# Performance work log

Measured on AMD Instinct MI355X. Metric: run time of the kernel, lower is better.

## Reference

```python
import jax, jax.numpy as jnp
import numpy as np

N = 4096          # neurons (and input size)
T = 300           # timesteps = time / dt
DT = 1.0
TIME = 300.0
REST = 0.0
RESET = 0.0
THRESH = 10.0
REFRAC = 1.0
TC_DECAY = 100.0


def setup_inputs() -> dict:
    key = jax.random.key(0)
    k1, k2, k3 = jax.random.split(key, 3)
    inp = jax.random.randint(k1, (T, N), 0, 2).astype(jnp.int32)   # binary spike train
    w = jax.random.normal(k2, (N, N), jnp.float32) * 0.05
    w_rec = jax.random.normal(k3, (N, N), jnp.float32) * 0.05
    return {"inp": inp, "w": w, "w_rec": w_rec}


def _simulate(inp, w, w_rec):
    # Faithful port of LIFLayer.__call__ applied over T timesteps via lax.scan.
    # Per step (original order): x = inp@w + s_prev@w_rec; v = decay*(v-rest)+rest;
    # x[rt>0]=0; rt-=dt; v+=x; s=(v>=thresh); t[s]=ts*dt/time; rt[s]=refrac; v[s]=reset.
    decay = jnp.exp(jnp.float32(-DT / TC_DECAY))
    n = w.shape[1]
    v0 = jnp.full((n,), RESET, jnp.float32)
    rt0 = jnp.zeros((n,), jnp.float32)
    s0 = jnp.zeros((n,), jnp.float32)   # previous-step spikes (s[:, -1])
    t0 = jnp.ones((n,), jnp.float32)    # t initialized to ones (store_all_spikes=False)

    def step(carry, xs):
        v, rt, s_prev, t_prev = carry
        inp_t, ts = xs
        x = inp_t.astype(jnp.float32) @ w + s_prev @ w_rec   # [n]
        v = decay * (v - REST) + REST                        # v_ext = 0 (default)
        x = jnp.where(rt > 0, jnp.float32(0.0), x)           # refractory gating
        rt = rt - DT
        v = v + x
        spike = v >= THRESH
        s = spike.astype(jnp.float32)
        t_new = jnp.where(spike, ts.astype(jnp.float32) * DT / TIME, t_prev)
        rt = jnp.where(spike, jnp.float32(REFRAC), rt)
        v = jnp.where(spike, jnp.float32(RESET), v)
        return (v, rt, s, t_new), (s, t_new, v)

    _, (s_all, t_all, v_all) = jax.lax.scan(
        step, (v0, rt0, s0, t0), (inp, jnp.arange(inp.shape[0]))
    )
    return s_all, t_all, v_all


def reference(inp, w, w_rec):
    # Returns per-timestep spikes [T,n], spike-time record [T,n], and membrane
    # potential trace [T,n] (post-reset v, the internal state the kernel computes).
    return _simulate(inp, w, w_rec)
```

## Files before the change

### kernel.cpp

```cpp
#include <hip/hip_runtime.h>
#include <hip/hip_cooperative_groups.h>

namespace cg = cooperative_groups;

#define NN    4096
#define TT    300
#define TPAD  320
#define TCH   20
#define GRID  256
#define BLOCK 1024
#define NREP  16
#define WSTRIDE 18
#define HROWS 2048
#define DECAYF 0.9900498337491681f
#define THRESHF 10.0f

#define WLDS_BYTES (HROWS * WSTRIDE * 4)
#define DSM_BYTES  (WLDS_BYTES + 2 * 16 * 17 * 4)

#define WS_REQ ((size_t)NN*TPAD*4*2 + (size_t)NREP*2*256*4)

__device__ __forceinline__ uint4 llc_load_v4(const uint4* p) {
    uint4 r;
    asm volatile("global_load_dwordx4 %0, %1, off sc0 sc1\n\t"
                 "s_waitcnt vmcnt(0)"
                 : "=v"(r) : "v"(p) : "memory");
    return r;
}

__global__ __launch_bounds__(BLOCK, 4)
void lif_sim(const int* __restrict__ inp, const float* __restrict__ w,
             const float* __restrict__ w_rec, float* __restrict__ out,
             float* __restrict__ ws)
{
    float* inpT = ws;
    float* X    = ws + (size_t)NN * TPAD;
    unsigned int* maskrep = (unsigned int*)(X + (size_t)TPAD * NN);

    float* s_all = out;
    float* t_all = out + (size_t)TT * NN;
    float* v_all = out + (size_t)2 * TT * NN;

    cg::grid_group grid = cg::this_grid();
    const int tid  = threadIdx.x;
    const int bid  = blockIdx.x;
    const int gtid = bid * BLOCK + tid;

    extern __shared__ __align__(16) unsigned char dsm[];
    float*        smem    = (float*)dsm;
    float*        wlds    = (float*)dsm;
    float*        red_sh  = (float*)(dsm + WLDS_BYTES);

    if (gtid < NREP * 2 * 256) maskrep[gtid] = 0u;
    if (gtid < NN * 32) {
        int j = gtid >> 5, tl = gtid & 31;
        if (tl < TPAD - TT) inpT[(size_t)j * TPAD + TT + tl] = 0.0f;
    }
    for (int idx = gtid; idx < TT * NN; idx += GRID * BLOCK) {
        int t = idx >> 12, j = idx & (NN - 1);
        inpT[(size_t)j * TPAD + t] = (float)inp[idx];
    }
    grid.sync();

    {
        const int ct  = bid >> 4;
        const int cc  = bid & 15;
        const int c1  = tid & 255;
        const int jp  = tid >> 8;
        const int col = cc * 256 + c1;
        const int t0  = ct * TCH;
        const int j0  = jp * 1024;
        const float* wp = w + col;
        float acc[20];
#pragma unroll
        for (int k = 0; k < 20; ++k) acc[k] = 0.0f;
        for (int j = j0; j < j0 + 1024; ++j) {
            float wj = wp[(size_t)j * NN];
            const float* iprow = inpT + (size_t)j * TPAD + t0;
#pragma unroll
            for (int k = 0; k < 20; ++k) acc[k] = fmaf(iprow[k], wj, acc[k]);
        }
#pragma unroll
        for (int half = 0; half < 2; ++half) {
#pragma unroll
            for (int k = 0; k < 10; ++k) smem[(jp * 10 + k) * 256 + c1] = acc[half * 10 + k];
            __syncthreads();
            if (jp == 0) {
#pragma unroll
                for (int k = 0; k < 10; ++k) {
                    float s = smem[k * 256 + c1] + smem[(10 + k) * 256 + c1]
                            + smem[(20 + k) * 256 + c1] + smem[(30 + k) * 256 + c1];
                    X[(size_t)(t0 + half * 10 + k) * NN + col] = s;
                }
            }
            __syncthreads();
        }
    }
    grid.sync();

    const int colgrp = ((bid & 7) << 5) | (bid >> 3);
    const int col0   = colgrp * 16;
    const int lane = tid & 63;
    const int wave = tid >> 6;
    const int c    = tid & 15;
    const int r    = tid >> 4;
    const int col  = col0 + c;

    {
        const int srow = tid >> 2;
        const int c4   = (tid & 3) << 2;
#pragma unroll
        for (int pass = 0; pass < 8; ++pass) {
            const int row = pass * 256 + srow;
            const float4 q = *(const float4*)(w_rec + (size_t)row * NN + col0 + c4);
            float2* dst = (float2*)(wlds + row * WSTRIDE + c4);
            dst[0] = make_float2(q.x, q.y);
            dst[1] = make_float2(q.z, q.w);
        }
    }
    __syncthreads();

    float v = 0.0f, tv = 1.0f;
    int sprev = 0;
    const float* wrc = w_rec + col + (size_t)(r << 6) * NN;
    const int ldsbase = (r << 6) * WSTRIDE + c;
    unsigned int* myrep = maskrep + ((bid & 15) * 2) * 256;

    float xreg = 0.0f;
    if (tid < 16) xreg = X[col];

    for (int t = 0; t < TT; ++t) {
        const uint4* pp = (const uint4*)(myrep + (t & 1) * 256) + r;
        const unsigned int ut = (unsigned int)t;
        uint4 q;
        for (;;) {
            q = llc_load_v4(pp);
            unsigned int bad = ((q.x >> 16) ^ ut) | ((q.y >> 16) ^ ut)
                             | ((q.z >> 16) ^ ut) | ((q.w >> 16) ^ ut);
            if (__all(bad == 0u)) break;
        }
        unsigned long long M = ((unsigned long long)(q.x & 0xFFFFu))
                             | ((unsigned long long)(q.y & 0xFFFFu) << 16)
                             | ((unsigned long long)(q.z & 0xFFFFu) << 32)
                             | ((unsigned long long)(q.w & 0xFFFFu) << 48);

        float acc0 = 0.0f, acc1 = 0.0f, acc2 = 0.0f, acc3 = 0.0f;
        if (r < 32) {
            while (M) {
                float l0, l1 = 0.0f, l2 = 0.0f, l3 = 0.0f;
                int b0 = __builtin_ctzll(M); M &= M - 1;
                l0 = wlds[ldsbase + b0 * WSTRIDE];
                if (M) { int b = __builtin_ctzll(M); M &= M - 1; l1 = wlds[ldsbase + b * WSTRIDE]; }
                if (M) { int b = __builtin_ctzll(M); M &= M - 1; l2 = wlds[ldsbase + b * WSTRIDE]; }
                if (M) { int b = __builtin_ctzll(M); M &= M - 1; l3 = wlds[ldsbase + b * WSTRIDE]; }
                acc0 += l0 + l2; acc1 += l1 + l3;
            }
        } else {
            while (M) {
                float l0,        l1 = 0.0f, l2 = 0.0f, l3 = 0.0f,
                      l4 = 0.0f, l5 = 0.0f, l6 = 0.0f, l7 = 0.0f,
                      l8 = 0.0f, l9 = 0.0f, l10 = 0.0f, l11 = 0.0f,
                      l12 = 0.0f, l13 = 0.0f, l14 = 0.0f, l15 = 0.0f;
                int b0 = __builtin_ctzll(M); M &= M - 1;
                l0 = wrc[(size_t)b0 * NN];
                if (M) { int b = __builtin_ctzll(M); M &= M - 1; l1  = wrc[(size_t)b * NN]; }
                if (M) { int b = __builtin_ctzll(M); M &= M - 1; l2  = wrc[(size_t)b * NN]; }
                if (M) { int b = __builtin_ctzll(M); M &= M - 1; l3  = wrc[(size_t)b * NN]; }
                if (M) { int b = __builtin_ctzll(M); M &= M - 1; l4  = wrc[(size_t)b * NN]; }
                if (M) { int b = __builtin_ctzll(M); M &= M - 1; l5  = wrc[(size_t)b * NN]; }
                if (M) { int b = __builtin_ctzll(M); M &= M - 1; l6  = wrc[(size_t)b * NN]; }
                if (M) { int b = __builtin_ctzll(M); M &= M - 1; l7  = wrc[(size_t)b * NN]; }
                if (M) { int b = __builtin_ctzll(M); M &= M - 1; l8  = wrc[(size_t)b * NN]; }
                if (M) { int b = __builtin_ctzll(M); M &= M - 1; l9  = wrc[(size_t)b * NN]; }
                if (M) { int b = __builtin_ctzll(M); M &= M - 1; l10 = wrc[(size_t)b * NN]; }
                if (M) { int b = __builtin_ctzll(M); M &= M - 1; l11 = wrc[(size_t)b * NN]; }
                if (M) { int b = __builtin_ctzll(M); M &= M - 1; l12 = wrc[(size_t)b * NN]; }
                if (M) { int b = __builtin_ctzll(M); M &= M - 1; l13 = wrc[(size_t)b * NN]; }
                if (M) { int b = __builtin_ctzll(M); M &= M - 1; l14 = wrc[(size_t)b * NN]; }
                if (M) { int b = __builtin_ctzll(M); M &= M - 1; l15 = wrc[(size_t)b * NN]; }
                acc0 += l0 + l4;  acc1 += l1 + l5;  acc2 += l2 + l6;  acc3 += l3 + l7;
                acc0 += l8 + l12; acc1 += l9 + l13; acc2 += l10 + l14; acc3 += l11 + l15;
            }
        }
        float part = (acc0 + acc1) + (acc2 + acc3);
        part += __shfl_xor(part, 16, 64);
        part += __shfl_xor(part, 32, 64);
        float* red = red_sh + (t & 1) * (16 * 17);
        if (lane < 16) red[wave * 17 + lane] = part;
        __syncthreads();

        if (wave == 0) {
            const int cw = lane & 15, h = lane >> 4;
            const float* sp = red + h * 4 * 17 + cw;
            float s = (sp[0] + sp[17]) + (sp[34] + sp[51]);
            s += __shfl_xor(s, 16, 64);
            s += __shfl_xor(s, 32, 64);

            bool spike = false;
            if (lane < 16) {
                float x = xreg + s;
                v *= DECAYF;
                if (sprev) x = 0.0f;
                v += x;
                spike = v >= THRESHF;
                if (spike) { tv = (float)t * (1.0f / 300.0f); v = 0.0f; }
                sprev = spike ? 1 : 0;
            }
            unsigned long long bal = __ballot(spike);
            unsigned int word = ((unsigned int)(t + 1) << 16)
                              | (unsigned int)(bal & 0xFFFFull);
            const int par = (t + 1) & 1;
            if (lane < NREP)
                __hip_atomic_store(maskrep + (lane * 2 + par) * 256 + colgrp, word,
                                   __ATOMIC_RELAXED, __HIP_MEMORY_SCOPE_AGENT);
            if (lane < 16) {
                size_t o = (size_t)t * NN + col;
                __builtin_nontemporal_store(spike ? 1.0f : 0.0f, &s_all[o]);
                __builtin_nontemporal_store(tv, &t_all[o]);
                __builtin_nontemporal_store(v, &v_all[o]);
                if (t + 1 < TT)
                    xreg = __builtin_nontemporal_load(&X[(size_t)(t + 1) * NN + col]);
            }
        }
    }
}

extern "C" void kernel_launch(void* const* d_in, const int* in_sizes, int n_in,
                              void* d_out, int out_size, void* d_ws, size_t ws_size,
                              hipStream_t stream) {
    if (ws_size < WS_REQ) return;
    const int*   inp   = (const int*)d_in[0];
    const float* w     = (const float*)d_in[1];
    const float* w_rec = (const float*)d_in[2];
    float* out = (float*)d_out;
    float* ws  = (float*)d_ws;
    hipFuncSetAttribute((const void*)lif_sim,
                        hipFuncAttributeMaxDynamicSharedMemorySize, DSM_BYTES);
    void* args[] = {(void*)&inp, (void*)&w, (void*)&w_rec, (void*)&out, (void*)&ws};
    hipLaunchCooperativeKernel((const void*)lif_sim, dim3(GRID), dim3(BLOCK),
                               args, DSM_BYTES, stream);
}
```

Before: 2.008 ms.

## Poll spike mask with one wave and broadcast via LDS; unroll LDS gather

Only wave 0 now spins on the replicated spike-mask words in the last-level cache and copies them to shared memory, followed by a block barrier. The other 15 waves no longer issue their own polling loads, which cuts memory traffic and contention on the flag lines. This adds a __syncthreads per step and single-buffers the reduction scratch. The change also raises wave 0's priority during the spike/flag-publish section, replaces the agent-scope atomic store with an sc0 sc1 store, and widens the LDS gather unroll from 4 to 8.

```diff
diff --git a/kernel.cpp b/kernel.cpp
--- a/kernel.cpp
+++ b/kernel.cpp
@@ -16,7 +16,7 @@
 #define THRESHF 10.0f
 
 #define WLDS_BYTES (HROWS * WSTRIDE * 4)
-#define DSM_BYTES  (WLDS_BYTES + 2 * 16 * 17 * 4)
+#define DSM_BYTES  (WLDS_BYTES + 1024 + 16 * 17 * 4)
 
 #define WS_REQ ((size_t)NN*TPAD*4*2 + (size_t)NREP*2*256*4)
 
@@ -26,6 +26,11 @@
                  "s_waitcnt vmcnt(0)"
                  : "=v"(r) : "v"(p) : "memory");
     return r;
+}
+
+__device__ __forceinline__ void llc_store_u32(unsigned int* p, unsigned int v) {
+    asm volatile("global_store_dword %0, %1, off sc0 sc1"
+                 :: "v"(p), "v"(v) : "memory");
 }
 
 __global__ __launch_bounds__(BLOCK, 4)
@@ -49,7 +54,8 @@
     extern __shared__ __align__(16) unsigned char dsm[];
     float*        smem    = (float*)dsm;
     float*        wlds    = (float*)dsm;
-    float*        red_sh  = (float*)(dsm + WLDS_BYTES);
+    unsigned int* mask_sh = (unsigned int*)(dsm + WLDS_BYTES);
+    float*        red_sh  = (float*)(dsm + WLDS_BYTES + 1024);
 
     if (gtid < NREP * 2 * 256) maskrep[gtid] = 0u;
     if (gtid < NN * 32) {
@@ -130,30 +136,43 @@
     if (tid < 16) xreg = X[col];
 
     for (int t = 0; t < TT; ++t) {
-        const uint4* pp = (const uint4*)(myrep + (t & 1) * 256) + r;
-        const unsigned int ut = (unsigned int)t;
-        uint4 q;
-        for (;;) {
-            q = llc_load_v4(pp);
-            unsigned int bad = ((q.x >> 16) ^ ut) | ((q.y >> 16) ^ ut)
-                             | ((q.z >> 16) ^ ut) | ((q.w >> 16) ^ ut);
-            if (__all(bad == 0u)) break;
-        }
-        unsigned long long M = ((unsigned long long)(q.x & 0xFFFFu))
-                             | ((unsigned long long)(q.y & 0xFFFFu) << 16)
-                             | ((unsigned long long)(q.z & 0xFFFFu) << 32)
-                             | ((unsigned long long)(q.w & 0xFFFFu) << 48);
-
+        if (wave == 0) {
+            const uint4* pp = (const uint4*)(myrep + (t & 1) * 256) + lane;
+            const unsigned int ut = (unsigned int)t;
+            uint4 q;
+            for (;;) {
+                q = llc_load_v4(pp);
+                unsigned int bad = ((q.x >> 16) ^ ut) | ((q.y >> 16) ^ ut)
+                                 | ((q.z >> 16) ^ ut) | ((q.w >> 16) ^ ut);
+                if (__all(bad == 0u)) break;
+            }
+            ((uint4*)mask_sh)[lane] = q;
+        }
+        __syncthreads();
+
+        unsigned long long M;
+        {
+            const unsigned int* ms = mask_sh + (r << 2);
+            M = ((unsigned long long)(ms[0] & 0xFFFFu))
+              | ((unsigned long long)(ms[1] & 0xFFFFu) << 16)
+              | ((unsigned long long)(ms[2] & 0xFFFFu) << 32)
+              | ((unsigned long long)(ms[3] & 0xFFFFu) << 48);
+        }
         float acc0 = 0.0f, acc1 = 0.0f, acc2 = 0.0f, acc3 = 0.0f;
         if (r < 32) {
             while (M) {
-                float l0, l1 = 0.0f, l2 = 0.0f, l3 = 0.0f;
+                float l0, l1 = 0.0f, l2 = 0.0f, l3 = 0.0f,
+                      l4 = 0.0f, l5 = 0.0f, l6 = 0.0f, l7 = 0.0f;
                 int b0 = __builtin_ctzll(M); M &= M - 1;
                 l0 = wlds[ldsbase + b0 * WSTRIDE];
                 if (M) { int b = __builtin_ctzll(M); M &= M - 1; l1 = wlds[ldsbase + b * WSTRIDE]; }
                 if (M) { int b = __builtin_ctzll(M); M &= M - 1; l2 = wlds[ldsbase + b * WSTRIDE]; }
                 if (M) { int b = __builtin_ctzll(M); M &= M - 1; l3 = wlds[ldsbase + b * WSTRIDE]; }
-                acc0 += l0 + l2; acc1 += l1 + l3;
+                if (M) { int b = __builtin_ctzll(M); M &= M - 1; l4 = wlds[ldsbase + b * WSTRIDE]; }
+                if (M) { int b = __builtin_ctzll(M); M &= M - 1; l5 = wlds[ldsbase + b * WSTRIDE]; }
+                if (M) { int b = __builtin_ctzll(M); M &= M - 1; l6 = wlds[ldsbase + b * WSTRIDE]; }
+                if (M) { int b = __builtin_ctzll(M); M &= M - 1; l7 = wlds[ldsbase + b * WSTRIDE]; }
+                acc0 += l0 + l4; acc1 += l1 + l5; acc2 += l2 + l6; acc3 += l3 + l7;
             }
         } else {
             while (M) {
@@ -185,13 +204,13 @@
         float part = (acc0 + acc1) + (acc2 + acc3);
         part += __shfl_xor(part, 16, 64);
         part += __shfl_xor(part, 32, 64);
-        float* red = red_sh + (t & 1) * (16 * 17);
-        if (lane < 16) red[wave * 17 + lane] = part;
+        if (lane < 16) red_sh[wave * 17 + lane] = part;
         __syncthreads();
 
         if (wave == 0) {
+            __builtin_amdgcn_s_setprio(1);
             const int cw = lane & 15, h = lane >> 4;
-            const float* sp = red + h * 4 * 17 + cw;
+            const float* sp = red_sh + h * 4 * 17 + cw;
             float s = (sp[0] + sp[17]) + (sp[34] + sp[51]);
             s += __shfl_xor(s, 16, 64);
             s += __shfl_xor(s, 32, 64);
@@ -211,8 +230,8 @@
                               | (unsigned int)(bal & 0xFFFFull);
             const int par = (t + 1) & 1;
             if (lane < NREP)
-                __hip_atomic_store(maskrep + (lane * 2 + par) * 256 + colgrp, word,
-                                   __ATOMIC_RELAXED, __HIP_MEMORY_SCOPE_AGENT);
+                llc_store_u32(maskrep + (lane * 2 + par) * 256 + colgrp, word);
+            __builtin_amdgcn_s_setprio(0);
             if (lane < 16) {
                 size_t o = (size_t)t * NN + col;
                 __builtin_nontemporal_store(spike ? 1.0f : 0.0f, &s_all[o]);
```

Result: faster. 1.699 ms (-15.4%).
